# Optimization experiments

Measured on AMD Instinct MI355X. Metric: run time of the kernel, lower is better.

## Reference

```python
import jax, jax.numpy as jnp
import numpy as np

N = 100000      # total nodes = B_GRAPHS * NODES_PER_GRAPH
NPG = 1000      # nodes per graph (num_nodes in module)
B_GRAPHS = 100
H = 128         # hidden_channels
CIN = 3         # in_channels
E = 1600000     # edges (avg_degree 16)
OUT = 2         # out_channels


def setup_inputs() -> dict:
    key = jax.random.key(0)
    ks = jax.random.split(key, 20)
    s = 0.05
    inp = {
        "x": jax.random.normal(ks[0], (N, CIN), jnp.float32),
        "edge_index": jnp.stack([
            jax.random.randint(ks[1], (E,), 0, N),
            jax.random.randint(ks[2], (E,), 0, N),
        ]).astype(jnp.int64),
        "batch": jnp.repeat(jnp.arange(B_GRAPHS), NPG).astype(jnp.int64),
        # DiffusionConv layer 0: CIN -> H ; layer 1: H -> H
        "W_self0": jax.random.normal(ks[3], (CIN, H), jnp.float32) * s,
        "W_nbr0": jax.random.normal(ks[4], (CIN, H), jnp.float32) * s,
        "b0": jnp.zeros((H,), jnp.float32),
        "W_self1": jax.random.normal(ks[5], (H, H), jnp.float32) * s,
        "W_nbr1": jax.random.normal(ks[6], (H, H), jnp.float32) * s,
        "b1": jnp.zeros((H,), jnp.float32),
        # 2 stacked LSTMs (torch layout: W_ih [4H, in], W_hh [4H, H])
        "Wih0": jax.random.normal(ks[7], (4 * H, H), jnp.float32) * s,
        "Whh0": jax.random.normal(ks[8], (4 * H, H), jnp.float32) * s,
        "bih0": jnp.zeros((4 * H,), jnp.float32),
        "bhh0": jnp.zeros((4 * H,), jnp.float32),
        "Wih1": jax.random.normal(ks[9], (4 * H, H), jnp.float32) * s,
        "Whh1": jax.random.normal(ks[10], (4 * H, H), jnp.float32) * s,
        "bih1": jnp.zeros((4 * H,), jnp.float32),
        "bhh1": jnp.zeros((4 * H,), jnp.float32),
        # output head
        "W_out": jax.random.normal(ks[11], (H, OUT), jnp.float32) * s,
        "b_out": jnp.zeros((OUT,), jnp.float32),
    }
    return inp


def diffusion_conv(h, src, dst, W_self, W_nbr, b):
    # gather-aggregate-transform: out = h W_self + (D^-1 A h) W_nbr + b
    msgs = h[src]                                            # [E, C] gather
    agg = jax.ops.segment_sum(msgs, dst, num_segments=N)     # [N, C] scatter-add
    deg = jax.ops.segment_sum(jnp.ones((src.shape[0], 1), h.dtype), dst,
                              num_segments=N)                # [N, 1]
    agg = agg / jnp.maximum(deg, 1.0)
    return h @ W_self + agg @ W_nbr + b


def lstm_layer(x_seq, Wih, Whh, bih, bhh):
    # x_seq: [T, Bn, H] seq-first, zero initial state (torch default)
    Bn = x_seq.shape[1]
    h0 = jnp.zeros((Bn, H), x_seq.dtype)
    c0 = jnp.zeros((Bn, H), x_seq.dtype)

    def step(carry, xt):
        h, c = carry
        g = xt @ Wih.T + h @ Whh.T + (bih + bhh)   # [Bn, 4H]
        i, f, gg, o = jnp.split(g, 4, axis=-1)     # torch gate order i,f,g,o
        c = jax.nn.sigmoid(f) * c + jax.nn.sigmoid(i) * jnp.tanh(gg)
        h = jax.nn.sigmoid(o) * jnp.tanh(c)
        return (h, c), h

    _, hs = jax.lax.scan(step, (h0, c0), x_seq)
    return hs


def reference(x, edge_index, batch, W_self0, W_nbr0, b0, W_self1, W_nbr1, b1,
              Wih0, Whh0, bih0, bhh0, Wih1, Whh1, bih1, bhh1, W_out, b_out):
    src, dst = edge_index[0], edge_index[1]
    h = jax.nn.relu(diffusion_conv(x, src, dst, W_self0, W_nbr0, b0))
    h = jax.nn.relu(diffusion_conv(h, src, dst, W_self1, W_nbr1, b1))
    # view(-1, num_nodes, hidden): [B_GRAPHS, NPG, H], LSTM seq-first
    seq = h.reshape(B_GRAPHS, NPG, H)
    seq = lstm_layer(seq, Wih0, Whh0, bih0, bhh0)
    seq = lstm_layer(seq, Wih1, Whh1, bih1, bhh1)
    h = seq.reshape(N, H)
    # global_mean_pool over batch vector
    pooled = jax.ops.segment_sum(h, batch, num_segments=B_GRAPHS)
    cnt = jax.ops.segment_sum(jnp.ones((N, 1), h.dtype), batch,
                              num_segments=B_GRAPHS)
    pooled = pooled / jnp.maximum(cnt, 1.0)
    logits = pooled @ W_out + b_out                # [B_GRAPHS, OUT]
    return jax.nn.log_softmax(logits, axis=1)
```

## Files before the change

kernel.cpp:

```cpp
#include <hip/hip_runtime.h>

#define N_NODES 100000
#define NPG     1000
#define B_GR    100
#define HDIM    128
#define E_EDGES 1600000

typedef __attribute__((ext_vector_type(8))) short bf16x8;
typedef __attribute__((ext_vector_type(4))) float f32x4;
typedef unsigned long long u64;

__device__ __forceinline__ float sigf(float x) { return 1.f / (1.f + __expf(-x)); }
__device__ __forceinline__ float tanh_fast(float x) { return 1.f - 2.f / (__expf(2.f * x) + 1.f); }
__device__ __forceinline__ unsigned short f2bf(float f) {
    unsigned u = __float_as_uint(f);
    unsigned r = (u + 0x7fffu + ((u >> 16) & 1u)) >> 16;
    return (unsigned short)r;
}

__global__ void k_count(const int* __restrict__ dst, int* __restrict__ cnt) {
    int e = blockIdx.x * 256 + threadIdx.x;
    if (e < E_EDGES) atomicAdd(&cnt[dst[e]], 1);
}

__global__ void k_scan1(const int* __restrict__ cnt, int* __restrict__ row_ptr, int* __restrict__ bsum) {
    __shared__ int sd[256];
    int tid = threadIdx.x;
    int base = blockIdx.x * 1024 + tid * 4;
    int v[4];
#pragma unroll
    for (int j = 0; j < 4; ++j) {
        int i = base + j;
        v[j] = (i < N_NODES) ? cnt[i] : 0;
    }
    int s = v[0] + v[1] + v[2] + v[3];
    sd[tid] = s;
    __syncthreads();
    for (int off = 1; off < 256; off <<= 1) {
        int t = (tid >= off) ? sd[tid - off] : 0;
        __syncthreads();
        sd[tid] += t;
        __syncthreads();
    }
    int excl = sd[tid] - s;
    int run = excl;
#pragma unroll
    for (int j = 0; j < 4; ++j) {
        int i = base + j;
        run += v[j];
        if (i < N_NODES) row_ptr[1 + i] = run;
    }
    if (tid == 255) bsum[blockIdx.x] = sd[255];
}

__global__ void k_scan2(int* __restrict__ bsum, int nb) {
    if (threadIdx.x == 0 && blockIdx.x == 0) {
        int carry = 0;
        for (int b = 0; b < nb; ++b) {
            int t = bsum[b];
            bsum[b] = carry;
            carry += t;
        }
    }
}

__global__ void k_scan3(int* __restrict__ row_ptr, const int* __restrict__ bsum, int* __restrict__ cursor) {
    int i = blockIdx.x * 256 + threadIdx.x;
    if (i >= N_NODES) return;
    int incl = row_ptr[1 + i] + bsum[i >> 10];
    row_ptr[1 + i] = incl;
    if (i == 0) { row_ptr[0] = 0; cursor[0] = 0; }
    if (i + 1 < N_NODES) cursor[i + 1] = incl;
}

__global__ void k_fill(const int* __restrict__ src, const int* __restrict__ dst,
                       int* __restrict__ cursor, int* __restrict__ csr_src) {
    int e = blockIdx.x * 256 + threadIdx.x;
    if (e >= E_EDGES) return;
    int d = dst[e];
    int pos = atomicAdd(&cursor[d], 1);
    csr_src[pos] = src[e];
}

__global__ void k_conv0(const float* __restrict__ x, const int* __restrict__ rp, const int* __restrict__ csr,
                        const float* __restrict__ Ws, const float* __restrict__ Wn, const float* __restrict__ b,
                        float* __restrict__ out) {
    int n = blockIdx.x;
    int tid = threadIdx.x;
    __shared__ float sagg[3];
    if (tid < 3) sagg[tid] = 0.f;
    __syncthreads();
    int s0 = rp[n], s1 = rp[n + 1];
    int deg = s1 - s0;
    for (int j = tid; j < deg; j += 128) {
        int s = csr[s0 + j];
        atomicAdd(&sagg[0], x[s * 3 + 0]);
        atomicAdd(&sagg[1], x[s * 3 + 1]);
        atomicAdd(&sagg[2], x[s * 3 + 2]);
    }
    __syncthreads();
    float inv = 1.f / fmaxf((float)deg, 1.f);
    float a0 = sagg[0] * inv, a1 = sagg[1] * inv, a2 = sagg[2] * inv;
    float x0 = x[n * 3 + 0], x1 = x[n * 3 + 1], x2 = x[n * 3 + 2];
    float acc = b[tid]
        + x0 * Ws[0 * 128 + tid] + x1 * Ws[1 * 128 + tid] + x2 * Ws[2 * 128 + tid]
        + a0 * Wn[0 * 128 + tid] + a1 * Wn[1 * 128 + tid] + a2 * Wn[2 * 128 + tid];
    out[n * 128 + tid] = fmaxf(acc, 0.f);
}

__global__ void k_agg(const float* __restrict__ hin, const int* __restrict__ rp, const int* __restrict__ csr,
                      float* __restrict__ out) {
    int n = blockIdx.x;
    int tid = threadIdx.x;
    __shared__ int sidx[128];
    int s0 = rp[n], s1 = rp[n + 1];
    int deg = s1 - s0;
    float acc = 0.f;
    for (int base = 0; base < deg; base += 128) {
        int m = min(128, deg - base);
        if (tid < m) sidx[tid] = csr[s0 + base + tid];
        __syncthreads();
        for (int j = 0; j < m; ++j) acc += hin[sidx[j] * 128 + tid];
        __syncthreads();
    }
    out[n * 128 + tid] = acc / fmaxf((float)deg, 1.f);
}

__global__ __launch_bounds__(256)
void k_conv1mm(const float* __restrict__ A, float* __restrict__ B,
               const float* __restrict__ Wself, const float* __restrict__ Wnbr,
               const float* __restrict__ bias) {
    __shared__ float As[64 * 64];
    __shared__ float Wls[64 * 128];
    int tid = threadIdx.x;
    int r0 = blockIdx.x * 64;
    int tx = tid & 31, ty = tid >> 5;
    float acc[8][4];
#pragma unroll
    for (int r = 0; r < 8; ++r)
#pragma unroll
        for (int j = 0; j < 4; ++j) acc[r][j] = 0.f;

    for (int chunk = 0; chunk < 4; ++chunk) {
        const float* Asrc = (chunk < 2) ? A : B;
        const float* Wsrc = (chunk < 2) ? Wself : Wnbr;
        int k0 = (chunk & 1) * 64;
#pragma unroll
        for (int i = 0; i < 4; ++i) {
            int e = tid + 256 * i;
            int row = e >> 4, c4 = e & 15;
            int grow = r0 + row;
            float4 v = make_float4(0.f, 0.f, 0.f, 0.f);
            if (grow < N_NODES) v = *(const float4*)&Asrc[grow * 128 + k0 + c4 * 4];
            *(float4*)&As[row * 64 + c4 * 4] = v;
        }
#pragma unroll
        for (int i = 0; i < 8; ++i) {
            int e = tid + 256 * i;
            int row = e >> 5, c4 = e & 31;
            *(float4*)&Wls[row * 128 + c4 * 4] = *(const float4*)&Wsrc[(k0 + row) * 128 + c4 * 4];
        }
        __syncthreads();
#pragma unroll 4
        for (int kk = 0; kk < 64; ++kk) {
            float4 w = *(const float4*)&Wls[kk * 128 + tx * 4];
#pragma unroll
            for (int r = 0; r < 8; ++r) {
                float a = As[(ty + 8 * r) * 64 + kk];
                acc[r][0] += a * w.x; acc[r][1] += a * w.y;
                acc[r][2] += a * w.z; acc[r][3] += a * w.w;
            }
        }
        __syncthreads();
    }
    float4 bb = *(const float4*)&bias[tx * 4];
#pragma unroll
    for (int r = 0; r < 8; ++r) {
        int grow = r0 + ty + 8 * r;
        if (grow < N_NODES) {
            float4 v;
            v.x = fmaxf(acc[r][0] + bb.x, 0.f);
            v.y = fmaxf(acc[r][1] + bb.y, 0.f);
            v.z = fmaxf(acc[r][2] + bb.z, 0.f);
            v.w = fmaxf(acc[r][3] + bb.w, 0.f);
            *(float4*)&B[grow * 128 + tx * 4] = v;
        }
    }
}

__global__ void k_prepf(const float* __restrict__ Wih0, const float* __restrict__ Whh0,
                        const float* __restrict__ Wih1, const float* __restrict__ Whh1,
                        unsigned short* __restrict__ WTf) {
    int idx = blockIdx.x * 256 + threadIdx.x;
    int lane = idx & 63;
    int gt = (idx >> 6) & 3;
    int kt = (idx >> 8) & 7;
    int w  = (idx >> 11) & 7;
    int l  = idx >> 14;
    int d = 16 * w + (lane & 15);
    int k0 = kt * 32 + (lane >> 4) * 8;
    int wrow = gt * 128 + d;
    const float* Wi = l ? Wih1 : Wih0;
    const float* Wh = l ? Whh1 : Whh0;
    const float* srcp = (k0 < 128) ? (Wi + wrow * 128 + k0) : (Wh + wrow * 128 + (k0 - 128));
    unsigned short o[8];
#pragma unroll
    for (int j = 0; j < 8; ++j) o[j] = f2bf(srcp[j]);
    u64 lo = (u64)o[0] | ((u64)o[1] << 16) | ((u64)o[2] << 32) | ((u64)o[3] << 48);
    u64 hi = (u64)o[4] | ((u64)o[5] << 16) | ((u64)o[6] << 32) | ((u64)o[7] << 48);
    u64* dst = (u64*)(WTf + (size_t)idx * 8);
    dst[0] = lo; dst[1] = hi;
}

__global__ void k_bsum(const float* __restrict__ bih0, const float* __restrict__ bhh0,
                       const float* __restrict__ bih1, const float* __restrict__ bhh1,
                       float* __restrict__ bs) {
    int i = blockIdx.x * 256 + threadIdx.x;
    int l = i >> 9, c = i & 511;
    bs[i] = l ? (bih1[c] + bhh1[c]) : (bih0[c] + bhh0[c]);
}

__global__ __launch_bounds__(512, 2)
void k_lstm_layer(const float* __restrict__ X32,
                  const unsigned short* __restrict__ Xf,
                  const unsigned short* __restrict__ WTf,
                  const float* __restrict__ bsL,
                  unsigned short* __restrict__ Hf_out,
                  float* __restrict__ pooled,
                  int mode) {
    __shared__ __align__(16) unsigned short xs[2048];
    __shared__ __align__(16) unsigned short hs[2048];
    int tid = threadIdx.x;
    int l = tid & 63;
    int w = tid >> 6;
    int rb = blockIdx.x;
    int n0 = rb * 16;
    int nreal = (n0 + 16 <= NPG) ? 16 : (NPG - n0);

    bf16x8 Bw[8][4];
    const bf16x8* Wv = (const bf16x8*)WTf;
#pragma unroll
    for (int kt = 0; kt < 8; ++kt)
#pragma unroll
        for (int gt = 0; gt < 4; ++gt)
            Bw[kt][gt] = Wv[((w * 8 + kt) * 4 + gt) * 64 + l];

    int d = (w << 4) | (l & 15);
    float bi = bsL[d], bf_ = bsL[128 + d], bg = bsL[256 + d], bo = bsL[384 + d];
    float cst0 = 0.f, cst1 = 0.f, cst2 = 0.f, cst3 = 0.f;

    int ktp = d >> 5, oct = (d >> 3) & 3, boff = d & 7;
    int hbase = ktp * 512 + ((l >> 4) * 4 + 16 * oct) * 8 + boff;

    ((u64*)hs)[tid] = 0ull;
    __syncthreads();

    for (int t = 0; t < 100; ++t) {
        if (mode == 0) {
            int r = tid & 15, g = tid >> 4;
            int row = n0 + r;
            f32x4 v = {0.f, 0.f, 0.f, 0.f};
            if (row < NPG) v = *(const f32x4*)(X32 + (size_t)(t * NPG + row) * 128 + g * 4);
            unsigned short h0 = f2bf(v.x), h1 = f2bf(v.y), h2 = f2bf(v.z), h3 = f2bf(v.w);
            u64 pk = (u64)h0 | ((u64)h1 << 16) | ((u64)h2 << 32) | ((u64)h3 << 48);
            int dd = g * 4;
            int hw = (dd >> 5) * 512 + (r + 16 * ((dd >> 3) & 3)) * 8 + (dd & 7);
            *(u64*)(xs + hw) = pk;
        } else {
            const u64* srcp = (const u64*)(Xf + (size_t)(t * 63 + rb) * 2048);
            ((u64*)xs)[tid] = srcp[tid];
        }
        __syncthreads();

        f32x4 acc[4];
#pragma unroll
        for (int gt = 0; gt < 4; ++gt) acc[gt] = (f32x4){0.f, 0.f, 0.f, 0.f};
#pragma unroll
        for (int kt = 0; kt < 8; ++kt) {
            const unsigned short* base = (kt < 4) ? xs : hs;
            bf16x8 a = *(const bf16x8*)(base + (kt & 3) * 512 + l * 8);
            acc[0] = __builtin_amdgcn_mfma_f32_16x16x32_bf16(a, Bw[kt][0], acc[0], 0, 0, 0);
            acc[1] = __builtin_amdgcn_mfma_f32_16x16x32_bf16(a, Bw[kt][1], acc[1], 0, 0, 0);
            acc[2] = __builtin_amdgcn_mfma_f32_16x16x32_bf16(a, Bw[kt][2], acc[2], 0, 0, 0);
            acc[3] = __builtin_amdgcn_mfma_f32_16x16x32_bf16(a, Bw[kt][3], acc[3], 0, 0, 0);
        }
        __syncthreads();

        float hsum = 0.f;
#pragma unroll
        for (int reg = 0; reg < 4; ++reg) {
            float gi = acc[0][reg] + bi;
            float gf = acc[1][reg] + bf_;
            float gg = acc[2][reg] + bg;
            float go = acc[3][reg] + bo;
            float cprev = (reg == 0) ? cst0 : (reg == 1) ? cst1 : (reg == 2) ? cst2 : cst3;
            float c = sigf(gf) * cprev + sigf(gi) * tanh_fast(gg);
            if (reg == 0) cst0 = c; else if (reg == 1) cst1 = c; else if (reg == 2) cst2 = c; else cst3 = c;
            float h = sigf(go) * tanh_fast(c);
            unsigned short hb = f2bf(h);
            hs[hbase + reg * 8] = hb;
            if (mode == 0) {
                Hf_out[(size_t)(t * 63 + rb) * 2048 + hbase + reg * 8] = hb;
            } else {
                int row = (l >> 4) * 4 + reg;
                if (row < nreal) hsum += h;
            }
        }
        if (mode == 1) {
            hsum += __shfl_xor(hsum, 16);
            hsum += __shfl_xor(hsum, 32);
            if ((l >> 4) == 0) atomicAdd(&pooled[t * 128 + d], hsum);
        }
        __syncthreads();
    }
}

__global__ void k_head(const float* __restrict__ pooled, const float* __restrict__ Wout,
                       const float* __restrict__ bout, float* __restrict__ out) {
    int gi = threadIdx.x;
    if (gi >= B_GR) return;
    float l0 = bout[0], l1 = bout[1];
    for (int d = 0; d < 128; ++d) {
        float p = pooled[gi * 128 + d] / 1000.0f;
        l0 += p * Wout[d * 2 + 0];
        l1 += p * Wout[d * 2 + 1];
    }
    float m = fmaxf(l0, l1);
    float lse = m + logf(__expf(l0 - m) + __expf(l1 - m));
    out[gi * 2 + 0] = l0 - lse;
    out[gi * 2 + 1] = l1 - lse;
}

extern "C" void kernel_launch(void* const* d_in, const int* in_sizes, int n_in,
                              void* d_out, int out_size, void* d_ws, size_t ws_size,
                              hipStream_t stream) {
    const float* x    = (const float*)d_in[0];
    const int*   ei   = (const int*)d_in[1];
    const int*   srcI = ei;
    const int*   dstI = ei + E_EDGES;
    const float* Ws0  = (const float*)d_in[3];
    const float* Wn0  = (const float*)d_in[4];
    const float* b0   = (const float*)d_in[5];
    const float* Ws1  = (const float*)d_in[6];
    const float* Wn1  = (const float*)d_in[7];
    const float* b1   = (const float*)d_in[8];
    const float* Wih0 = (const float*)d_in[9];
    const float* Whh0 = (const float*)d_in[10];
    const float* bih0 = (const float*)d_in[11];
    const float* bhh0 = (const float*)d_in[12];
    const float* Wih1 = (const float*)d_in[13];
    const float* Whh1 = (const float*)d_in[14];
    const float* bih1 = (const float*)d_in[15];
    const float* bhh1 = (const float*)d_in[16];
    const float* Wout = (const float*)d_in[17];
    const float* bout = (const float*)d_in[18];
    float* out = (float*)d_out;

    char* ws = (char*)d_ws;
    int*   row_ptr = (int*)(ws + 0);
    int*   cursor  = (int*)(ws + 400128);
    int*   csr_src = (int*)(ws + 800128);
    int*   bsum    = (int*)(ws + 7200128);
    float* bufA    = (float*)(ws + 7200640);
    float* bufB    = (float*)(ws + 58400640);
    unsigned short* WTf = (unsigned short*)(ws + 109600640);
    float* bsB     = (float*)(ws + 110649216);
    float* pooled  = (float*)(ws + 110653312);

    unsigned short* H0f = (unsigned short*)bufA;

    hipMemsetAsync(cursor, 0, N_NODES * sizeof(int), stream);
    hipMemsetAsync(pooled, 0, B_GR * 128 * sizeof(float), stream);

    k_count<<<E_EDGES / 256, 256, 0, stream>>>(dstI, cursor);
    k_scan1<<<98, 256, 0, stream>>>(cursor, row_ptr, bsum);
    k_scan2<<<1, 64, 0, stream>>>(bsum, 98);
    k_scan3<<<(N_NODES + 255) / 256, 256, 0, stream>>>(row_ptr, bsum, cursor);
    k_fill<<<E_EDGES / 256, 256, 0, stream>>>(srcI, dstI, cursor, csr_src);

    k_conv0<<<N_NODES, 128, 0, stream>>>(x, row_ptr, csr_src, Ws0, Wn0, b0, bufA);
    k_agg<<<N_NODES, 128, 0, stream>>>(bufA, row_ptr, csr_src, bufB);
    k_conv1mm<<<(N_NODES + 63) / 64, 256, 0, stream>>>(bufA, bufB, Ws1, Wn1, b1);

    k_prepf<<<128, 256, 0, stream>>>(Wih0, Whh0, Wih1, Whh1, WTf);
    k_bsum<<<4, 256, 0, stream>>>(bih0, bhh0, bih1, bhh1, bsB);

    k_lstm_layer<<<63, 512, 0, stream>>>(bufB, nullptr, WTf, bsB, H0f, nullptr, 0);
    k_lstm_layer<<<63, 512, 0, stream>>>(nullptr, H0f, WTf + 131072, bsB + 512, nullptr, pooled, 1);

    k_head<<<1, 128, 0, stream>>>(pooled, Wout, bout, out);
}
```

Baseline: 1.007 ms.

## Warp-per-node aggregation, pre-packed bf16 LSTM inputs, and pipelined LSTM recurrence

```diff
diff --git a/kernel.cpp b/kernel.cpp
--- a/kernel.cpp
+++ b/kernel.cpp
@@ -9,14 +9,19 @@
 typedef __attribute__((ext_vector_type(8))) short bf16x8;
 typedef __attribute__((ext_vector_type(4))) float f32x4;
 typedef unsigned long long u64;
+typedef unsigned short u16;
 
 __device__ __forceinline__ float sigf(float x) { return 1.f / (1.f + __expf(-x)); }
 __device__ __forceinline__ float tanh_fast(float x) { return 1.f - 2.f / (__expf(2.f * x) + 1.f); }
-__device__ __forceinline__ unsigned short f2bf(float f) {
+__device__ __forceinline__ u16 f2bf(float f) {
     unsigned u = __float_as_uint(f);
     unsigned r = (u + 0x7fffu + ((u >> 16) & 1u)) >> 16;
-    return (unsigned short)r;
-}
+    return (u16)r;
+}
+__device__ __forceinline__ f32x4 MF(bf16x8 a, bf16x8 b, f32x4 c) {
+    return __builtin_amdgcn_mfma_f32_16x16x32_bf16(a, b, c, 0, 0, 0);
+}
+#define BAR() asm volatile("s_waitcnt lgkmcnt(0)\n\ts_barrier" ::: "memory")
 
 __global__ void k_count(const int* __restrict__ dst, int* __restrict__ cnt) {
     int e = blockIdx.x * 256 + threadIdx.x;
@@ -108,22 +113,43 @@
     out[n * 128 + tid] = fmaxf(acc, 0.f);
 }
 
-__global__ void k_agg(const float* __restrict__ hin, const int* __restrict__ rp, const int* __restrict__ csr,
-                      float* __restrict__ out) {
-    int n = blockIdx.x;
-    int tid = threadIdx.x;
-    __shared__ int sidx[128];
-    int s0 = rp[n], s1 = rp[n + 1];
-    int deg = s1 - s0;
-    float acc = 0.f;
-    for (int base = 0; base < deg; base += 128) {
-        int m = min(128, deg - base);
-        if (tid < m) sidx[tid] = csr[s0 + base + tid];
-        __syncthreads();
-        for (int j = 0; j < m; ++j) acc += hin[sidx[j] * 128 + tid];
-        __syncthreads();
-    }
-    out[n * 128 + tid] = acc / fmaxf((float)deg, 1.f);
+__global__ __launch_bounds__(256)
+void k_agg2(const float* __restrict__ hin, const int* __restrict__ rp, const int* __restrict__ csr,
+            float* __restrict__ out) {
+    int wid = threadIdx.x >> 6;
+    int l = threadIdx.x & 63;
+    int n = blockIdx.x * 4 + wid;
+    if (n >= N_NODES) return;
+    int s0 = rp[n], deg = rp[n + 1] - s0;
+    float ax = 0.f, ay = 0.f;
+    const float2* base = (const float2*)hin;
+    for (int c0 = 0; c0 < deg; c0 += 64) {
+        int m = min(64, deg - c0);
+        int myidx = csr[s0 + c0 + ((l < m) ? l : 0)];
+        int j = 0;
+        for (; j + 4 <= m; j += 4) {
+            int i0 = __shfl(myidx, j);
+            int i1 = __shfl(myidx, j + 1);
+            int i2 = __shfl(myidx, j + 2);
+            int i3 = __shfl(myidx, j + 3);
+            float2 v0 = base[(size_t)i0 * 64 + l];
+            float2 v1 = base[(size_t)i1 * 64 + l];
+            float2 v2 = base[(size_t)i2 * 64 + l];
+            float2 v3 = base[(size_t)i3 * 64 + l];
+            ax += v0.x; ay += v0.y;
+            ax += v1.x; ay += v1.y;
+            ax += v2.x; ay += v2.y;
+            ax += v3.x; ay += v3.y;
+        }
+        for (; j < m; ++j) {
+            int i0 = __shfl(myidx, j);
+            float2 v = base[(size_t)i0 * 64 + l];
+            ax += v.x; ay += v.y;
+        }
+    }
+    float dv = fmaxf((float)deg, 1.f);
+    float2 o; o.x = ax / dv; o.y = ay / dv;
+    *(float2*)&out[(size_t)n * 128 + l * 2] = o;
 }
 
 __global__ __launch_bounds__(256)
@@ -188,9 +214,27 @@
     }
 }
 
+__global__ void k_tobf16(const float* __restrict__ C, u16* __restrict__ Xf) {
+    int g = blockIdx.x * 256 + threadIdx.x;
+    int vr = g >> 5;
+    int c4 = g & 31;
+    int t = vr / 1008;
+    int rv = vr - t * 1008;
+    int r = min(rv, NPG - 1);
+    int n = t * NPG + r;
+    int col0 = c4 * 4;
+    f32x4 v = *(const f32x4*)(C + (size_t)n * 128 + col0);
+    u16 h0 = f2bf(v[0]), h1 = f2bf(v[1]), h2 = f2bf(v[2]), h3 = f2bf(v[3]);
+    u64 pk = (u64)h0 | ((u64)h1 << 16) | ((u64)h2 << 32) | ((u64)h3 << 48);
+    int rb = rv >> 4, rr = rv & 15;
+    size_t idx = (size_t)(t * 63 + rb) * 2048
+               + (size_t)((col0 >> 5) * 512 + ((col0 >> 3) & 3) * 128 + rr * 8 + (col0 & 7));
+    *(u64*)(Xf + idx) = pk;
+}
+
 __global__ void k_prepf(const float* __restrict__ Wih0, const float* __restrict__ Whh0,
                         const float* __restrict__ Wih1, const float* __restrict__ Whh1,
-                        unsigned short* __restrict__ WTf) {
+                        u16* __restrict__ WTf) {
     int idx = blockIdx.x * 256 + threadIdx.x;
     int lane = idx & 63;
     int gt = (idx >> 6) & 3;
@@ -203,13 +247,12 @@
     const float* Wi = l ? Wih1 : Wih0;
     const float* Wh = l ? Whh1 : Whh0;
     const float* srcp = (k0 < 128) ? (Wi + wrow * 128 + k0) : (Wh + wrow * 128 + (k0 - 128));
-    unsigned short o[8];
+    u16 o[8];
 #pragma unroll
     for (int j = 0; j < 8; ++j) o[j] = f2bf(srcp[j]);
-    u64 lo = (u64)o[0] | ((u64)o[1] << 16) | ((u64)o[2] << 32) | ((u64)o[3] << 48);
-    u64 hi = (u64)o[4] | ((u64)o[5] << 16) | ((u64)o[6] << 32) | ((u64)o[7] << 48);
     u64* dst = (u64*)(WTf + (size_t)idx * 8);
-    dst[0] = lo; dst[1] = hi;
+    dst[0] = (u64)o[0] | ((u64)o[1] << 16) | ((u64)o[2] << 32) | ((u64)o[3] << 48);
+    dst[1] = (u64)o[4] | ((u64)o[5] << 16) | ((u64)o[6] << 32) | ((u64)o[7] << 48);
 }
 
 __global__ void k_bsum(const float* __restrict__ bih0, const float* __restrict__ bhh0,
@@ -220,25 +263,76 @@
     bs[i] = l ? (bih1[c] + bhh1[c]) : (bih0[c] + bhh0[c]);
 }
 
-__global__ __launch_bounds__(512, 2)
-void k_lstm_layer(const float* __restrict__ X32,
-                  const unsigned short* __restrict__ Xf,
-                  const unsigned short* __restrict__ WTf,
-                  const float* __restrict__ bsL,
-                  unsigned short* __restrict__ Hf_out,
-                  float* __restrict__ pooled,
-                  int mode) {
-    __shared__ __align__(16) unsigned short xs[2048];
-    __shared__ __align__(16) unsigned short hs[2048];
+#define LSTM_STEP(ACC, ACCN, T, CUR)                                                   \
+    do {                                                                               \
+        BAR();                                                                         \
+        _Pragma("unroll")                                                              \
+        for (int kt = 0; kt < 4; ++kt) {                                               \
+            bf16x8 af = *(const bf16x8*)(hsh[CUR] + kt * 512 + l * 8);                 \
+            ACC[0] = MF(af, Bw[4 + kt][0], ACC[0]);                                    \
+            ACC[1] = MF(af, Bw[4 + kt][1], ACC[1]);                                    \
+            ACC[2] = MF(af, Bw[4 + kt][2], ACC[2]);                                    \
+            ACC[3] = MF(af, Bw[4 + kt][3], ACC[3]);                                    \
+        }                                                                              \
+        if (mode == 0 && (T) > 0)                                                      \
+            ((u64*)(Hout + (size_t)(((T) - 1) * 63 + rb) * 2048))[tid] =               \
+                ((const u64*)hsh[CUR])[tid];                                           \
+        if ((T) < 99) {                                                                \
+            _Pragma("unroll")                                                          \
+            for (int g = 0; g < 4; ++g) ACCN[g] = (f32x4){0.f, 0.f, 0.f, 0.f};         \
+            _Pragma("unroll")                                                          \
+            for (int kt = 0; kt < 4; ++kt) {                                           \
+                ACCN[0] = MF(xf[kt], Bw[kt][0], ACCN[0]);                              \
+                ACCN[1] = MF(xf[kt], Bw[kt][1], ACCN[1]);                              \
+                ACCN[2] = MF(xf[kt], Bw[kt][2], ACCN[2]);                              \
+                ACCN[3] = MF(xf[kt], Bw[kt][3], ACCN[3]);                              \
+            }                                                                          \
+        }                                                                              \
+        if ((T) < 98) {                                                                \
+            const u16* xn = xbase + (size_t)((T) + 2) * TSTR;                          \
+            _Pragma("unroll")                                                          \
+            for (int kt = 0; kt < 4; ++kt)                                             \
+                xf[kt] = *(const bf16x8*)(xn + kt * 512);                              \
+        }                                                                              \
+        float hsum = 0.f;                                                              \
+        _Pragma("unroll")                                                              \
+        for (int reg = 0; reg < 4; ++reg) {                                            \
+            float gi = ACC[0][reg] + bi;                                               \
+            float gf = ACC[1][reg] + bf_;                                              \
+            float gg = ACC[2][reg] + bg;                                               \
+            float go = ACC[3][reg] + bo;                                               \
+            float cprev = (reg == 0) ? cst0 : (reg == 1) ? cst1 : (reg == 2) ? cst2 : cst3; \
+            float c = sigf(gf) * cprev + sigf(gi) * tanh_fast(gg);                     \
+            if (reg == 0) cst0 = c; else if (reg == 1) cst1 = c;                       \
+            else if (reg == 2) cst2 = c; else cst3 = c;                                \
+            float h = sigf(go) * tanh_fast(c);                                         \
+            hsh[(CUR) ^ 1][hbase + reg * 8] = f2bf(h);                                 \
+            if (mode == 1) {                                                           \
+                int row = (l >> 4) * 4 + reg;                                          \
+                if (row < nreal) hsum += h;                                            \
+            }                                                                          \
+        }                                                                              \
+        if (mode == 1) {                                                               \
+            hsum += __shfl_xor(hsum, 16);                                              \
+            hsum += __shfl_xor(hsum, 32);                                              \
+            if ((l >> 4) == 0) atomicAdd(&pooled[(T) * 128 + d], hsum);                \
+        }                                                                              \
+    } while (0)
+
+__global__ __launch_bounds__(512)
+void k_lstm_layer(const u16* __restrict__ Xf, const u16* __restrict__ WTl,
+                  const float* __restrict__ bsL, u16* __restrict__ Hout,
+                  float* __restrict__ pooled, int mode) {
+    __shared__ __align__(16) u16 hsh[2][2048];
     int tid = threadIdx.x;
     int l = tid & 63;
     int w = tid >> 6;
     int rb = blockIdx.x;
     int n0 = rb * 16;
-    int nreal = (n0 + 16 <= NPG) ? 16 : (NPG - n0);
+    int nreal = min(16, NPG - n0);
 
     bf16x8 Bw[8][4];
-    const bf16x8* Wv = (const bf16x8*)WTf;
+    const bf16x8* Wv = (const bf16x8*)WTl;
 #pragma unroll
     for (int kt = 0; kt < 8; ++kt)
 #pragma unroll
@@ -252,67 +346,36 @@
     int ktp = d >> 5, oct = (d >> 3) & 3, boff = d & 7;
     int hbase = ktp * 512 + ((l >> 4) * 4 + 16 * oct) * 8 + boff;
 
-    ((u64*)hs)[tid] = 0ull;
-    __syncthreads();
-
-    for (int t = 0; t < 100; ++t) {
-        if (mode == 0) {
-            int r = tid & 15, g = tid >> 4;
-            int row = n0 + r;
-            f32x4 v = {0.f, 0.f, 0.f, 0.f};
-            if (row < NPG) v = *(const f32x4*)(X32 + (size_t)(t * NPG + row) * 128 + g * 4);
-            unsigned short h0 = f2bf(v.x), h1 = f2bf(v.y), h2 = f2bf(v.z), h3 = f2bf(v.w);
-            u64 pk = (u64)h0 | ((u64)h1 << 16) | ((u64)h2 << 32) | ((u64)h3 << 48);
-            int dd = g * 4;
-            int hw = (dd >> 5) * 512 + (r + 16 * ((dd >> 3) & 3)) * 8 + (dd & 7);
-            *(u64*)(xs + hw) = pk;
-        } else {
-            const u64* srcp = (const u64*)(Xf + (size_t)(t * 63 + rb) * 2048);
-            ((u64*)xs)[tid] = srcp[tid];
-        }
-        __syncthreads();
-
-        f32x4 acc[4];
-#pragma unroll
-        for (int gt = 0; gt < 4; ++gt) acc[gt] = (f32x4){0.f, 0.f, 0.f, 0.f};
-#pragma unroll
-        for (int kt = 0; kt < 8; ++kt) {
-            const unsigned short* base = (kt < 4) ? xs : hs;
-            bf16x8 a = *(const bf16x8*)(base + (kt & 3) * 512 + l * 8);
-            acc[0] = __builtin_amdgcn_mfma_f32_16x16x32_bf16(a, Bw[kt][0], acc[0], 0, 0, 0);
-            acc[1] = __builtin_amdgcn_mfma_f32_16x16x32_bf16(a, Bw[kt][1], acc[1], 0, 0, 0);
-            acc[2] = __builtin_amdgcn_mfma_f32_16x16x32_bf16(a, Bw[kt][2], acc[2], 0, 0, 0);
-            acc[3] = __builtin_amdgcn_mfma_f32_16x16x32_bf16(a, Bw[kt][3], acc[3], 0, 0, 0);
-        }
-        __syncthreads();
-
-        float hsum = 0.f;
-#pragma unroll
-        for (int reg = 0; reg < 4; ++reg) {
-            float gi = acc[0][reg] + bi;
-            float gf = acc[1][reg] + bf_;
-            float gg = acc[2][reg] + bg;
-            float go = acc[3][reg] + bo;
-            float cprev = (reg == 0) ? cst0 : (reg == 1) ? cst1 : (reg == 2) ? cst2 : cst3;
-            float c = sigf(gf) * cprev + sigf(gi) * tanh_fast(gg);
-            if (reg == 0) cst0 = c; else if (reg == 1) cst1 = c; else if (reg == 2) cst2 = c; else cst3 = c;
-            float h = sigf(go) * tanh_fast(c);
-            unsigned short hb = f2bf(h);
-            hs[hbase + reg * 8] = hb;
-            if (mode == 0) {
-                Hf_out[(size_t)(t * 63 + rb) * 2048 + hbase + reg * 8] = hb;
-            } else {
-                int row = (l >> 4) * 4 + reg;
-                if (row < nreal) hsum += h;
-            }
-        }
-        if (mode == 1) {
-            hsum += __shfl_xor(hsum, 16);
-            hsum += __shfl_xor(hsum, 32);
-            if ((l >> 4) == 0) atomicAdd(&pooled[t * 128 + d], hsum);
-        }
-        __syncthreads();
-    }
+    const u16* xbase = Xf + (size_t)rb * 2048 + l * 8;
+    const size_t TSTR = (size_t)63 * 2048;
+
+    bf16x8 xf[4];
+#pragma unroll
+    for (int kt = 0; kt < 4; ++kt) xf[kt] = *(const bf16x8*)(xbase + kt * 512);
+
+    f32x4 accA[4], accB[4];
+#pragma unroll
+    for (int g = 0; g < 4; ++g) accA[g] = (f32x4){0.f, 0.f, 0.f, 0.f};
+#pragma unroll
+    for (int kt = 0; kt < 4; ++kt) {
+        accA[0] = MF(xf[kt], Bw[kt][0], accA[0]);
+        accA[1] = MF(xf[kt], Bw[kt][1], accA[1]);
+        accA[2] = MF(xf[kt], Bw[kt][2], accA[2]);
+        accA[3] = MF(xf[kt], Bw[kt][3], accA[3]);
+    }
+#pragma unroll
+    for (int kt = 0; kt < 4; ++kt) xf[kt] = *(const bf16x8*)(xbase + TSTR + kt * 512);
+
+    ((u64*)hsh[0])[tid] = 0ull;
+
+    for (int t2 = 0; t2 < 50; ++t2) {
+        int t0 = 2 * t2;
+        LSTM_STEP(accA, accB, t0, 0);
+        LSTM_STEP(accB, accA, t0 + 1, 1);
+    }
+    BAR();
+    if (mode == 0)
+        ((u64*)(Hout + (size_t)(99 * 63 + rb) * 2048))[tid] = ((const u64*)hsh[0])[tid];
 }
 
 __global__ void k_head(const float* __restrict__ pooled, const float* __restrict__ Wout,
@@ -363,11 +426,12 @@
     int*   bsum    = (int*)(ws + 7200128);
     float* bufA    = (float*)(ws + 7200640);
     float* bufB    = (float*)(ws + 58400640);
-    unsigned short* WTf = (unsigned short*)(ws + 109600640);
+    u16*   WTf     = (u16*)(ws + 109600640);
     float* bsB     = (float*)(ws + 110649216);
     float* pooled  = (float*)(ws + 110653312);
 
-    unsigned short* H0f = (unsigned short*)bufA;
+    u16* Xf  = (u16*)(ws + 7200640);
+    u16* H0f = (u16*)(ws + 33005440);
 
     hipMemsetAsync(cursor, 0, N_NODES * sizeof(int), stream);
     hipMemsetAsync(pooled, 0, B_GR * 128 * sizeof(float), stream);
@@ -379,14 +443,15 @@
     k_fill<<<E_EDGES / 256, 256, 0, stream>>>(srcI, dstI, cursor, csr_src);
 
     k_conv0<<<N_NODES, 128, 0, stream>>>(x, row_ptr, csr_src, Ws0, Wn0, b0, bufA);
-    k_agg<<<N_NODES, 128, 0, stream>>>(bufA, row_ptr, csr_src, bufB);
+    k_agg2<<<N_NODES / 4, 256, 0, stream>>>(bufA, row_ptr, csr_src, bufB);
     k_conv1mm<<<(N_NODES + 63) / 64, 256, 0, stream>>>(bufA, bufB, Ws1, Wn1, b1);
+    k_tobf16<<<12600, 256, 0, stream>>>(bufB, Xf);
 
     k_prepf<<<128, 256, 0, stream>>>(Wih0, Whh0, Wih1, Whh1, WTf);
     k_bsum<<<4, 256, 0, stream>>>(bih0, bhh0, bih1, bhh1, bsB);
 
-    k_lstm_layer<<<63, 512, 0, stream>>>(bufB, nullptr, WTf, bsB, H0f, nullptr, 0);
-    k_lstm_layer<<<63, 512, 0, stream>>>(nullptr, H0f, WTf + 131072, bsB + 512, nullptr, pooled, 1);
+    k_lstm_layer<<<63, 512, 0, stream>>>(Xf, WTf, bsB, H0f, nullptr, 0);
+    k_lstm_layer<<<63, 512, 0, stream>>>(H0f, WTf + 131072, bsB + 512, nullptr, pooled, 1);
 
     k_head<<<1, 128, 0, stream>>>(pooled, Wout, bout, out);
 }
```

After: 885.8 us. -12.1%, faster.
